# Kernel optimization log

Measured on AMD Instinct MI355X. Metric: run time of the kernel, lower is better.

Reference implementation:

```python
import jax, jax.numpy as jnp
import numpy as np


def setup_inputs() -> dict:
    key = jax.random.key(0)
    k1, k2 = jax.random.split(key)
    B, C, H, W = 8, 256, 64, 64
    x = jax.random.normal(k1, (B, C, H, W), dtype=jnp.float32)
    # gamma is a learned scalar (nn.Parameter(torch.zeros(1))); init nonzero
    # so the attention branch contributes to the output for testing.
    gamma = jax.random.normal(k2, (1,), dtype=jnp.float32)
    return {"x": x, "gamma": gamma}


def reference(x, gamma):
    B, C, H, W = x.shape
    f = x.reshape(B, C, H * W)  # (B, C, N) with N = H*W
    # attn[b, n, m] = softmax_m( sum_c f[b,c,n] * f[b,c,m] )  -- no scaling, per module
    scores = jnp.einsum('bcn,bcm->bnm', f, f)  # (B, N, N)
    attn = jax.nn.softmax(scores, axis=-1)
    # out[b, c, n] = sum_m f[b,c,m] * attn[b,n,m]   (bmm(d, attn^T))
    out = jnp.einsum('bcm,bnm->bcn', f, attn).reshape(B, C, H, W)
    return gamma * out + x
```

## Files before the change

### kernel.cpp

```cpp
#include <hip/hip_runtime.h>
#include <hip/hip_bf16.h>

typedef __attribute__((ext_vector_type(8))) short short8;
typedef __attribute__((ext_vector_type(4))) float f32x4;

#define NB 8
#define NC 256
#define NNN 4096

__device__ __forceinline__ ushort f2bf(float f) {
  __hip_bfloat16 h = __float2bfloat16(f);
  return *reinterpret_cast<ushort*>(&h);
}

__global__ __launch_bounds__(256) void prep_kernel(const float* __restrict__ x,
                                                   ushort* __restrict__ fT) {
  __shared__ float tile[32][33];
  const int tx = threadIdx.x, ty = threadIdx.y;
  const int n0 = blockIdx.x * 32, c0 = blockIdx.y * 32, b = blockIdx.z;
#pragma unroll
  for (int k = 0; k < 4; ++k) {
    tile[ty + 8 * k][tx] =
        x[((size_t)(b * NC + c0 + ty + 8 * k)) * NNN + n0 + tx];
  }
  __syncthreads();
#pragma unroll
  for (int k = 0; k < 4; ++k) {
    int n = n0 + ty + 8 * k;
    fT[((size_t)(b * NNN + n)) * NC + c0 + tx] = f2bf(tile[tx][ty + 8 * k]);
  }
}

__global__ __launch_bounds__(256, 2) void attn_kernel(
    const float* __restrict__ x, const ushort* __restrict__ fT,
    const float* __restrict__ gamma, float* __restrict__ out) {
  __shared__ union U {
    struct {
      ushort Kt[64][264];
      ushort Vt[256][72];
      ushort Pw[4][16][72];
    } a;
    float ot[4][256 * 17];
  } sm __attribute__((aligned(16)));

  const int tid = threadIdx.x;
  const int wave = tid >> 6;
  const int lane = tid & 63;
  const int g = lane >> 4;
  const int r = lane & 15;
  const int b = blockIdx.x & 7;
  const int n0 = (blockIdx.x >> 3) << 6;

  const ushort* fTb = fT + (size_t)b * NNN * NC;
  const float* xb = x + (size_t)b * NC * NNN;

  short8 q[8];
  {
    const ushort* qp = fTb + (size_t)(n0 + wave * 16 + r) * NC + 8 * g;
#pragma unroll
    for (int kf = 0; kf < 8; ++kf) q[kf] = *(const short8*)(qp + kf * 32);
  }

  f32x4 o[16];
#pragma unroll
  for (int cf = 0; cf < 16; ++cf) o[cf] = (f32x4){0.f, 0.f, 0.f, 0.f};
  float m_run[4] = {-3e38f, -3e38f, -3e38f, -3e38f};
  float l_run[4] = {0.f, 0.f, 0.f, 0.f};
  const float L2E = 1.44269504088896f;

  for (int mt = 0; mt < NNN / 64; ++mt) {
    const int m0 = mt * 64;
    __syncthreads();
    {
      const int row = tid >> 5;
      const int col = (tid & 31) * 8;
#pragma unroll
      for (int p = 0; p < 8; ++p)
        *(short8*)&sm.a.Kt[row + 8 * p][col] =
            *(const short8*)(fTb + (size_t)(m0 + row + 8 * p) * NC + col);
    }
    {
      const int row = tid >> 3;
      const int col = (tid & 7) * 8;
#pragma unroll
      for (int p = 0; p < 8; ++p) {
        const float* src = xb + (size_t)(row + 32 * p) * NNN + m0 + col;
        f32x4 v0 = *(const f32x4*)src;
        f32x4 v1 = *(const f32x4*)(src + 4);
        short8 w;
        w[0] = (short)f2bf(v0[0]); w[1] = (short)f2bf(v0[1]);
        w[2] = (short)f2bf(v0[2]); w[3] = (short)f2bf(v0[3]);
        w[4] = (short)f2bf(v1[0]); w[5] = (short)f2bf(v1[1]);
        w[6] = (short)f2bf(v1[2]); w[7] = (short)f2bf(v1[3]);
        *(short8*)&sm.a.Vt[row + 32 * p][col] = w;
      }
    }
    __syncthreads();

    f32x4 s[4];
#pragma unroll
    for (int mf = 0; mf < 4; ++mf) s[mf] = (f32x4){0.f, 0.f, 0.f, 0.f};
#pragma unroll
    for (int kc = 0; kc < 8; ++kc) {
#pragma unroll
      for (int mf = 0; mf < 4; ++mf) {
        short8 kb = *(const short8*)&sm.a.Kt[mf * 16 + r][kc * 32 + 8 * g];
        s[mf] = __builtin_amdgcn_mfma_f32_16x16x32_bf16(q[kc], kb, s[mf], 0, 0, 0);
      }
    }

    float scale[4], rsum[4];
#pragma unroll
    for (int i = 0; i < 4; ++i) {
      float rm = fmaxf(fmaxf(s[0][i], s[1][i]), fmaxf(s[2][i], s[3][i]));
#pragma unroll
      for (int off = 1; off < 16; off <<= 1)
        rm = fmaxf(rm, __shfl_xor(rm, off));
      float mn = fmaxf(m_run[i], rm);
      scale[i] = exp2f((m_run[i] - mn) * L2E);
      m_run[i] = mn;
      rsum[i] = 0.f;
    }
#pragma unroll
    for (int mf = 0; mf < 4; ++mf) {
#pragma unroll
      for (int i = 0; i < 4; ++i) {
        float p = exp2f((s[mf][i] - m_run[i]) * L2E);
        s[mf][i] = p;
        rsum[i] += p;
      }
    }
#pragma unroll
    for (int i = 0; i < 4; ++i) {
      float rs = rsum[i];
#pragma unroll
      for (int off = 1; off < 16; off <<= 1) rs += __shfl_xor(rs, off);
      l_run[i] = l_run[i] * scale[i] + rs;
    }
    f32x4 sc = (f32x4){scale[0], scale[1], scale[2], scale[3]};
#pragma unroll
    for (int cf = 0; cf < 16; ++cf) o[cf] *= sc;

#pragma unroll
    for (int mf = 0; mf < 4; ++mf)
#pragma unroll
      for (int i = 0; i < 4; ++i)
        sm.a.Pw[wave][4 * g + i][mf * 16 + r] = f2bf(s[mf][i]);

#pragma unroll
    for (int ks = 0; ks < 2; ++ks) {
      short8 pa = *(const short8*)&sm.a.Pw[wave][r][ks * 32 + 8 * g];
#pragma unroll
      for (int cf = 0; cf < 16; ++cf) {
        short8 vb = *(const short8*)&sm.a.Vt[cf * 16 + r][ks * 32 + 8 * g];
        o[cf] = __builtin_amdgcn_mfma_f32_16x16x32_bf16(pa, vb, o[cf], 0, 0, 0);
      }
    }
  }

  __syncthreads();

  float linv[4];
#pragma unroll
  for (int i = 0; i < 4; ++i) linv[i] = 1.0f / l_run[i];
  float* ot = sm.ot[wave];
#pragma unroll
  for (int cf = 0; cf < 16; ++cf)
#pragma unroll
    for (int i = 0; i < 4; ++i)
      ot[(cf * 16 + r) * 17 + 4 * g + i] = o[cf][i] * linv[i];
  const float gam = gamma[0];
#pragma unroll
  for (int k = 0; k < 16; ++k) {
    const int c = k * 16 + (lane >> 2);
    const int nn = (lane & 3) * 4;
    const size_t gi = ((size_t)(b * NC + c)) * NNN + n0 + wave * 16 + nn;
    f32x4 xv = *(const f32x4*)(x + gi);
    f32x4 ov;
#pragma unroll
    for (int j = 0; j < 4; ++j) ov[j] = ot[c * 17 + nn + j];
    *(f32x4*)(out + gi) = gam * ov + xv;
  }
}

extern "C" void kernel_launch(void* const* d_in, const int* in_sizes, int n_in,
                              void* d_out, int out_size, void* d_ws,
                              size_t ws_size, hipStream_t stream) {
  const float* x = (const float*)d_in[0];
  const float* gamma = (const float*)d_in[1];
  float* out = (float*)d_out;
  ushort* fT = (ushort*)d_ws;

  dim3 pg(NNN / 32, NC / 32, NB);
  dim3 pb(32, 8, 1);
  prep_kernel<<<pg, pb, 0, stream>>>(x, fT);

  attn_kernel<<<dim3(NB * (NNN / 64)), dim3(256), 0, stream>>>(x, fT, gamma, out);
}
```

Measured before the change: 298.6 us.

## Rewrite attention kernel with 32x32 MFMA, register prefetch, swizzled LDS, lazy rescale

The attention kernel is restructured to use 32x32x16 bf16 MFMA with 128 queries per block (32 per wave) and a grid of 256 blocks. K and V tiles are prefetched into registers for the next iteration while the current one computes, and they are stored to XOR-swizzled LDS so the separate padded arrays are no longer needed. P is moved between lanes with register shuffles instead of a round trip through LDS. The online softmax now keeps one running max per row and rescales only when the max grows by more than a threshold. Occupancy drops to one block per CU, and the output epilogue becomes scalar stores, which may reduce memory efficiency.

```diff
diff --git a/kernel.cpp b/kernel.cpp
--- a/kernel.cpp
+++ b/kernel.cpp
@@ -3,14 +3,20 @@
 
 typedef __attribute__((ext_vector_type(8))) short short8;
 typedef __attribute__((ext_vector_type(4))) float f32x4;
+typedef __attribute__((ext_vector_type(16))) float f32x16;
+typedef __attribute__((ext_vector_type(4))) unsigned int u32x4;
 
 #define NB 8
 #define NC 256
 #define NNN 4096
+#define L2E 1.44269504088896f
 
 __device__ __forceinline__ ushort f2bf(float f) {
   __hip_bfloat16 h = __float2bfloat16(f);
   return *reinterpret_cast<ushort*>(&h);
+}
+__device__ __forceinline__ unsigned pack2(float a, float b) {
+  return (unsigned)f2bf(a) | ((unsigned)f2bf(b) << 16);
 }
 
 __global__ __launch_bounds__(256) void prep_kernel(const float* __restrict__ x,
@@ -31,155 +37,197 @@
   }
 }
 
-__global__ __launch_bounds__(256, 2) void attn_kernel(
+__global__ __launch_bounds__(256, 1) void attn_kernel(
     const float* __restrict__ x, const ushort* __restrict__ fT,
     const float* __restrict__ gamma, float* __restrict__ out) {
-  __shared__ union U {
-    struct {
-      ushort Kt[64][264];
-      ushort Vt[256][72];
-      ushort Pw[4][16][72];
-    } a;
-    float ot[4][256 * 17];
-  } sm __attribute__((aligned(16)));
+  __shared__ __align__(16) char smem[66048];
 
   const int tid = threadIdx.x;
-  const int wave = tid >> 6;
-  const int lane = tid & 63;
-  const int g = lane >> 4;
-  const int r = lane & 15;
+  const int w = tid >> 6;
+  const int l = tid & 63;
+  const int l31 = l & 31;
+  const int h = l >> 5;
   const int b = blockIdx.x & 7;
-  const int n0 = (blockIdx.x >> 3) << 6;
+  const int gn0 = (blockIdx.x >> 3) * 128;
+  const int n0w = gn0 + w * 32;
 
   const ushort* fTb = fT + (size_t)b * NNN * NC;
   const float* xb = x + (size_t)b * NC * NNN;
 
-  short8 q[8];
+  short8 q[16];
   {
-    const ushort* qp = fTb + (size_t)(n0 + wave * 16 + r) * NC + 8 * g;
-#pragma unroll
-    for (int kf = 0; kf < 8; ++kf) q[kf] = *(const short8*)(qp + kf * 32);
-  }
-
-  f32x4 o[16];
-#pragma unroll
-  for (int cf = 0; cf < 16; ++cf) o[cf] = (f32x4){0.f, 0.f, 0.f, 0.f};
-  float m_run[4] = {-3e38f, -3e38f, -3e38f, -3e38f};
-  float l_run[4] = {0.f, 0.f, 0.f, 0.f};
-  const float L2E = 1.44269504088896f;
-
-  for (int mt = 0; mt < NNN / 64; ++mt) {
-    const int m0 = mt * 64;
-    __syncthreads();
-    {
-      const int row = tid >> 5;
-      const int col = (tid & 31) * 8;
-#pragma unroll
-      for (int p = 0; p < 8; ++p)
-        *(short8*)&sm.a.Kt[row + 8 * p][col] =
-            *(const short8*)(fTb + (size_t)(m0 + row + 8 * p) * NC + col);
-    }
-    {
-      const int row = tid >> 3;
-      const int col = (tid & 7) * 8;
-#pragma unroll
-      for (int p = 0; p < 8; ++p) {
-        const float* src = xb + (size_t)(row + 32 * p) * NNN + m0 + col;
-        f32x4 v0 = *(const f32x4*)src;
-        f32x4 v1 = *(const f32x4*)(src + 4);
-        short8 w;
-        w[0] = (short)f2bf(v0[0]); w[1] = (short)f2bf(v0[1]);
-        w[2] = (short)f2bf(v0[2]); w[3] = (short)f2bf(v0[3]);
-        w[4] = (short)f2bf(v1[0]); w[5] = (short)f2bf(v1[1]);
-        w[6] = (short)f2bf(v1[2]); w[7] = (short)f2bf(v1[3]);
-        *(short8*)&sm.a.Vt[row + 32 * p][col] = w;
+    const ushort* qp = fTb + (size_t)(n0w + l31) * NC + 8 * h;
+#pragma unroll
+    for (int kc = 0; kc < 16; ++kc) q[kc] = *(const short8*)(qp + kc * 16);
+  }
+
+  f32x16 o[8];
+#pragma unroll
+  for (int cf = 0; cf < 8; ++cf)
+#pragma unroll
+    for (int r = 0; r < 16; ++r) o[cf][r] = 0.f;
+  float m_run = -3.0e38f, l_run = 0.f;
+
+  short8 kreg[8];
+  f32x4 vreg[16];
+  const int km = tid & 63;
+#pragma unroll
+  for (int k = 0; k < 8; ++k)
+    kreg[k] = *(const short8*)(fTb + (size_t)km * NC + (w + 4 * k) * 8);
+#pragma unroll
+  for (int k = 0; k < 16; ++k)
+    vreg[k] = *(const f32x4*)(xb + (size_t)tid * NNN + 4 * k);
+
+  for (int t = 0; t < 64; ++t) {
+#pragma unroll
+    for (int k = 0; k < 8; ++k) {
+      const int byte = ((w + 4 * k) * 16) ^ ((km & 7) << 4);
+      *(short8*)(smem + km * 512 + byte) = kreg[k];
+    }
+#pragma unroll
+    for (int k = 0; k < 8; ++k) {
+      f32x4 a0 = vreg[2 * k], a1 = vreg[2 * k + 1];
+      short8 wv;
+      wv[0] = (short)f2bf(a0[0]); wv[1] = (short)f2bf(a0[1]);
+      wv[2] = (short)f2bf(a0[2]); wv[3] = (short)f2bf(a0[3]);
+      wv[4] = (short)f2bf(a1[0]); wv[5] = (short)f2bf(a1[1]);
+      wv[6] = (short)f2bf(a1[2]); wv[7] = (short)f2bf(a1[3]);
+      const int byte = (k * 16) ^ ((tid & 7) << 4);
+      *(short8*)(smem + 32768 + tid * 128 + byte) = wv;
+    }
+    __syncthreads();
+
+    if (t < 63) {
+      const int m0 = (t + 1) * 64;
+#pragma unroll
+      for (int k = 0; k < 8; ++k)
+        kreg[k] =
+            *(const short8*)(fTb + (size_t)(m0 + km) * NC + (w + 4 * k) * 8);
+#pragma unroll
+      for (int k = 0; k < 16; ++k)
+        vreg[k] = *(const f32x4*)(xb + (size_t)tid * NNN + m0 + 4 * k);
+    }
+
+    f32x16 s0, s1;
+#pragma unroll
+    for (int r = 0; r < 16; ++r) { s0[r] = 0.f; s1[r] = 0.f; }
+#pragma unroll
+    for (int kc = 0; kc < 16; ++kc) {
+      const int bb = (kc * 32 + 16 * h) ^ ((l31 & 7) << 4);
+      short8 ka0 = *(const short8*)(smem + l31 * 512 + bb);
+      short8 ka1 = *(const short8*)(smem + (32 + l31) * 512 + bb);
+      s0 = __builtin_amdgcn_mfma_f32_32x32x16_bf16(ka0, q[kc], s0, 0, 0, 0);
+      s1 = __builtin_amdgcn_mfma_f32_32x32x16_bf16(ka1, q[kc], s1, 0, 0, 0);
+    }
+
+    float tm = s0[0];
+#pragma unroll
+    for (int r = 1; r < 16; ++r) tm = fmaxf(tm, s0[r]);
+#pragma unroll
+    for (int r = 0; r < 16; ++r) tm = fmaxf(tm, s1[r]);
+    tm = fmaxf(tm, __shfl_xor(tm, 32));
+
+    if (__any(tm > m_run + 8.f)) {
+      const float mnew = fmaxf(m_run, tm);
+      const float alpha = exp2f((m_run - mnew) * L2E);
+      m_run = mnew;
+      l_run *= alpha;
+      float ar[16];
+#pragma unroll
+      for (int r = 0; r < 16; ++r)
+        ar[r] = __shfl(alpha, (r & 3) + 8 * (r >> 2) + 4 * h);
+#pragma unroll
+      for (int cf = 0; cf < 8; ++cf)
+#pragma unroll
+        for (int r = 0; r < 16; ++r) o[cf][r] *= ar[r];
+    }
+
+    float rsum = 0.f;
+#pragma unroll
+    for (int r = 0; r < 16; ++r) {
+      float p = exp2f((s0[r] - m_run) * L2E); s0[r] = p; rsum += p;
+    }
+#pragma unroll
+    for (int r = 0; r < 16; ++r) {
+      float p = exp2f((s1[r] - m_run) * L2E); s1[r] = p; rsum += p;
+    }
+    rsum += __shfl_xor(rsum, 32);
+    l_run += rsum;
+
+    unsigned d0[8], d1[8];
+#pragma unroll
+    for (int k = 0; k < 8; ++k) {
+      const int rg = 4 * (k >> 1) + 2 * (k & 1);
+      d0[k] = pack2(s0[rg], s0[rg + 1]);
+      d1[k] = pack2(s1[rg], s1[rg + 1]);
+    }
+    unsigned x0[4], x1[4];
+#pragma unroll
+    for (int j = 0; j < 4; ++j) {
+      const int iH1 = (j < 2) ? j : j + 2;
+      const int iH0 = (j < 2) ? j + 2 : j + 4;
+      unsigned s0v = h ? d0[iH1] : d0[iH0];
+      unsigned s1v = h ? d1[iH1] : d1[iH0];
+      x0[j] = (unsigned)__shfl_xor((int)s0v, 32);
+      x1[j] = (unsigned)__shfl_xor((int)s1v, 32);
+    }
+
+#pragma unroll
+    for (int ks = 0; ks < 4; ++ks) {
+      const int e = ks & 1;
+      unsigned fa0, fa1, fa2, fa3;
+      if (ks < 2) {
+        fa0 = h ? x0[2 * e] : d0[4 * e];
+        fa1 = h ? x0[2 * e + 1] : d0[4 * e + 1];
+        fa2 = h ? d0[4 * e + 2] : x0[2 * e];
+        fa3 = h ? d0[4 * e + 3] : x0[2 * e + 1];
+      } else {
+        fa0 = h ? x1[2 * e] : d1[4 * e];
+        fa1 = h ? x1[2 * e + 1] : d1[4 * e + 1];
+        fa2 = h ? d1[4 * e + 2] : x1[2 * e];
+        fa3 = h ? d1[4 * e + 3] : x1[2 * e + 1];
       }
-    }
-    __syncthreads();
-
-    f32x4 s[4];
-#pragma unroll
-    for (int mf = 0; mf < 4; ++mf) s[mf] = (f32x4){0.f, 0.f, 0.f, 0.f};
-#pragma unroll
-    for (int kc = 0; kc < 8; ++kc) {
-#pragma unroll
-      for (int mf = 0; mf < 4; ++mf) {
-        short8 kb = *(const short8*)&sm.a.Kt[mf * 16 + r][kc * 32 + 8 * g];
-        s[mf] = __builtin_amdgcn_mfma_f32_16x16x32_bf16(q[kc], kb, s[mf], 0, 0, 0);
+      u32x4 fu = {fa0, fa1, fa2, fa3};
+      short8 pa = __builtin_bit_cast(short8, fu);
+#pragma unroll
+      for (int cf = 0; cf < 8; ++cf) {
+        const int c = cf * 32 + l31;
+        const int byte = (ks * 32 + 16 * h) ^ ((c & 7) << 4);
+        short8 vb = *(const short8*)(smem + 32768 + c * 128 + byte);
+        o[cf] = __builtin_amdgcn_mfma_f32_32x32x16_bf16(pa, vb, o[cf], 0, 0, 0);
       }
     }
-
-    float scale[4], rsum[4];
-#pragma unroll
-    for (int i = 0; i < 4; ++i) {
-      float rm = fmaxf(fmaxf(s[0][i], s[1][i]), fmaxf(s[2][i], s[3][i]));
-#pragma unroll
-      for (int off = 1; off < 16; off <<= 1)
-        rm = fmaxf(rm, __shfl_xor(rm, off));
-      float mn = fmaxf(m_run[i], rm);
-      scale[i] = exp2f((m_run[i] - mn) * L2E);
-      m_run[i] = mn;
-      rsum[i] = 0.f;
-    }
-#pragma unroll
-    for (int mf = 0; mf < 4; ++mf) {
-#pragma unroll
-      for (int i = 0; i < 4; ++i) {
-        float p = exp2f((s[mf][i] - m_run[i]) * L2E);
-        s[mf][i] = p;
-        rsum[i] += p;
+    __syncthreads();
+  }
+
+  const float linv = 1.0f / l_run;
+  float lr[16];
+#pragma unroll
+  for (int r = 0; r < 16; ++r)
+    lr[r] = __shfl(linv, (r & 3) + 8 * (r >> 2) + 4 * h);
+  const float gam = gamma[0];
+  float* ot = (float*)smem + w * (32 * 129);
+#pragma unroll
+  for (int pass = 0; pass < 2; ++pass) {
+#pragma unroll
+    for (int cf = 0; cf < 4; ++cf) {
+      const int cfg = pass * 4 + cf;
+#pragma unroll
+      for (int r = 0; r < 16; ++r) {
+        const int nr = (r & 3) + 8 * (r >> 2) + 4 * h;
+        ot[nr * 129 + cf * 32 + l31] = o[cfg][r] * lr[r];
       }
     }
-#pragma unroll
-    for (int i = 0; i < 4; ++i) {
-      float rs = rsum[i];
-#pragma unroll
-      for (int off = 1; off < 16; off <<= 1) rs += __shfl_xor(rs, off);
-      l_run[i] = l_run[i] * scale[i] + rs;
-    }
-    f32x4 sc = (f32x4){scale[0], scale[1], scale[2], scale[3]};
-#pragma unroll
-    for (int cf = 0; cf < 16; ++cf) o[cf] *= sc;
-
-#pragma unroll
-    for (int mf = 0; mf < 4; ++mf)
-#pragma unroll
-      for (int i = 0; i < 4; ++i)
-        sm.a.Pw[wave][4 * g + i][mf * 16 + r] = f2bf(s[mf][i]);
-
-#pragma unroll
-    for (int ks = 0; ks < 2; ++ks) {
-      short8 pa = *(const short8*)&sm.a.Pw[wave][r][ks * 32 + 8 * g];
-#pragma unroll
-      for (int cf = 0; cf < 16; ++cf) {
-        short8 vb = *(const short8*)&sm.a.Vt[cf * 16 + r][ks * 32 + 8 * g];
-        o[cf] = __builtin_amdgcn_mfma_f32_16x16x32_bf16(pa, vb, o[cf], 0, 0, 0);
-      }
-    }
-  }
-
-  __syncthreads();
-
-  float linv[4];
-#pragma unroll
-  for (int i = 0; i < 4; ++i) linv[i] = 1.0f / l_run[i];
-  float* ot = sm.ot[wave];
-#pragma unroll
-  for (int cf = 0; cf < 16; ++cf)
-#pragma unroll
-    for (int i = 0; i < 4; ++i)
-      ot[(cf * 16 + r) * 17 + 4 * g + i] = o[cf][i] * linv[i];
-  const float gam = gamma[0];
-#pragma unroll
-  for (int k = 0; k < 16; ++k) {
-    const int c = k * 16 + (lane >> 2);
-    const int nn = (lane & 3) * 4;
-    const size_t gi = ((size_t)(b * NC + c)) * NNN + n0 + wave * 16 + nn;
-    f32x4 xv = *(const f32x4*)(x + gi);
-    f32x4 ov;
-#pragma unroll
-    for (int j = 0; j < 4; ++j) ov[j] = ot[c * 17 + nn + j];
-    *(f32x4*)(out + gi) = gam * ov + xv;
+    __syncthreads();
+#pragma unroll 8
+    for (int i = 0; i < 64; ++i) {
+      const int cl = 2 * i + h;
+      const float ov = ot[l31 * 129 + cl];
+      const size_t gi =
+          ((size_t)(b * NC + pass * 128 + cl)) * NNN + n0w + l31;
+      out[gi] = gam * ov + x[gi];
+    }
+    __syncthreads();
   }
 }
 
@@ -195,5 +243,5 @@
   dim3 pb(32, 8, 1);
   prep_kernel<<<pg, pb, 0, stream>>>(x, fT);
 
-  attn_kernel<<<dim3(NB * (NNN / 64)), dim3(256), 0, stream>>>(x, fT, gamma, out);
-}
+  attn_kernel<<<dim3(256), dim3(256), 0, stream>>>(x, fT, gamma, out);
+}
```

Measured after the change: 500.4 us. +67.6%, slower.
